# Performance work log

Hardware: AMD Instinct MI355X
Metric: run time of the kernel (lower is better)

Reference implementation:

```python
import math
import jax, jax.numpy as jnp
import numpy as np

# ---- hard-coded constants from the source module ----
T_H = 1.5; M = 60; DT = T_H / M; SQDT = math.sqrt(DT)
ALPHA = 0.8; RHO = 0.3; SQ1MR2 = math.sqrt(1.0 - RHO * RHO)
GAMMA = 5.0; KAPPA_Y = 1.2; LB_W = 1e-3
R = 0.02; SIGMA = 0.2; SIGMA_Y = 0.3; THETA_Y = 0.0; PI_CAP = 2.0
RPTS = 128       # sub_batch (one accumulation iteration)
REPEATS = 128    # total repeats == sub_batch -> single loop pass
N_PTS = 32       # number of eval states
HID = 64


def setup_inputs():
    key = jax.random.key(0)
    ks = jax.random.split(key, 8)
    W = 0.8 + 0.4 * jax.random.uniform(ks[0], (N_PTS, 1), jnp.float32)   # W0_range
    Y = -1.0 + 2.0 * jax.random.uniform(ks[1], (N_PTS, 1), jnp.float32)  # Y0_range
    TmT = jnp.full((N_PTS, 1), T_H, jnp.float32)
    B = RPTS * N_PTS
    # [sim(+/-), draw(z1/z2), step, path, 1] -- fresh noise per antithetic branch, as in torch
    noise = jax.random.normal(ks[2], (2, 2, M, B, 1), jnp.float32)
    w1 = 0.1 * jax.random.normal(ks[3], (3, HID), jnp.float32)
    b1 = jnp.zeros((HID,), jnp.float32)
    w2 = 0.1 * jax.random.normal(ks[4], (HID, HID), jnp.float32)
    b2 = jnp.zeros((HID,), jnp.float32)
    w3 = 0.1 * jax.random.normal(ks[5], (HID, 1), jnp.float32)
    b3 = jnp.zeros((1,), jnp.float32)
    return {"W": W, "TmT": TmT, "Y": Y, "noise": noise,
            "w1": w1, "b1": b1, "w2": w2, "b2": b2, "w3": w3, "b3": b3}


def _policy(params, W, TmT, Y):
    w1, b1, w2, b2, w3, b3 = params
    x = jnp.concatenate([W, TmT, Y], axis=-1)          # [B,3]
    h = jnp.tanh(x @ w1 + b1)
    h = jnp.tanh(h @ w2 + b2)
    return h @ w3 + b3                                 # [B,1]


def _simulate(params, W0, Y0, z1, z2, anti):
    """60-step Euler-Maruyama; returns CRRA utility U(W_T), shape [B,1]."""
    logW = jnp.log(jnp.clip(W0, LB_W, None))
    TmT0 = jnp.full_like(W0, T_H)

    def step(carry, zs):
        logW, Y, TmT = carry
        z1s, z2s = zs
        pi = _policy(params, jnp.exp(logW), TmT, Y)
        zW = anti * z1s
        zY = anti * (RHO * z1s + SQ1MR2 * z2s)
        drift = R + pi * (SIGMA * ALPHA * Y)
        var = (pi * SIGMA) ** 2
        logW = logW + (drift - 0.5 * var) * DT + pi * SIGMA * SQDT * zW
        Y = Y + KAPPA_Y * (THETA_Y - Y) * DT + SIGMA_Y * SQDT * zY
        logW = jnp.log(jnp.clip(jnp.exp(logW), LB_W, None))
        return (logW, Y, TmT - DT), None

    (logW, _, _), _ = jax.lax.scan(step, (logW, Y0, TmT0), (z1, z2))
    W_T = jnp.exp(logW)
    return W_T ** (1.0 - GAMMA) / (1.0 - GAMMA)        # gamma != 1


def reference(W, TmT, Y, noise, w1, b1, w2, b2, w3, b3):
    params = (w1, b1, w2, b2, w3, b3)
    n = W.shape[0]
    Wd = jax.lax.stop_gradient(W)   # forward detaches W, Y
    Yd = jax.lax.stop_gradient(Y)
    W0 = jnp.tile(Wd, (RPTS, 1))    # [B,1]
    Y0 = jnp.tile(Yd, (RPTS, 1))
    z1p, z2p = noise[0, 0], noise[0, 1]
    z1m, z2m = noise[1, 0], noise[1, 1]

    def f(W0_, Y0_):
        U = 0.5 * (_simulate(params, W0_, Y0_, z1p, z2p, 1.0)
                   + _simulate(params, W0_, Y0_, z1m, z2m, -1.0))
        # U_avg.sum() as in torch: mean over rpts, sum over eval points
        return jnp.sum(jnp.mean(U.reshape(RPTS, n), axis=0))

    lam_full = jax.grad(f, 0)(W0, Y0)                  # [B,1]

    def g(W0_, Y0_):
        # lam.view(rpts,n,1).mean(0).sum() == sum(lam_full)/rpts
        return jnp.sum(jax.grad(f, 0)(W0_, Y0_)) / RPTS

    dW_full, dY_full = jax.grad(g, (0, 1))(W0, Y0)     # [B,1] each

    inv = 1.0 / REPEATS   # faithful to source accumulation scaling
    lam = lam_full.reshape(RPTS, n, 1).mean(0) * inv
    dlamW = dW_full.reshape(RPTS, n, 1).mean(0) * inv
    dlamY = dY_full.reshape(RPTS, n, 1).mean(0) * inv

    # project_pmp
    mu_minus_r = SIGMA * (ALPHA * Yd)
    coeff = -1.0 / (Wd * dlamW + 1e-8)
    myo = coeff * (lam * (mu_minus_r / SIGMA ** 2))
    hedge = coeff * (SIGMA * RHO * SIGMA_Y * dlamY / SIGMA ** 2)
    return jnp.clip(myo + hedge, -PI_CAP, PI_CAP)      # [n,1]
```

## Files before the change

kernel.cpp:

```cpp
#include <hip/hip_runtime.h>
#include <math.h>

#define HID    64
#define MSTEPS 60
#define NPTS   32
#define RPTSC  128
#define BTOT   (RPTSC*NPTS)
#define NSIM   (2*BTOT)
#define NWAVE  (NSIM/2)

#define C_DT     0.025f
#define C_SQDT   0.15811388300841897f
#define C_ALPHA  0.8f
#define C_RHO    0.3f
#define C_SQ1MR2 0.9539392014169456f
#define C_KAPPA  1.2f
#define C_R      0.02f
#define C_SIGMA  0.2f
#define C_SIGY   0.3f
#define C_LBW    1e-3f
#define C_LOGLBW -6.907755279f

#define WAVE_LDS 3584
#define A_ROW    144
#define OFF_DV   2304
#define OFF_DA   3328

typedef _Float16 half8 __attribute__((ext_vector_type(8)));
typedef float    f32x4 __attribute__((ext_vector_type(4)));
typedef __fp16   fp16x2 __attribute__((ext_vector_type(2)));

__device__ __forceinline__ float rlanef(float v, int l) {
    return __int_as_float(__builtin_amdgcn_readlane(__float_as_int(v), l));
}
template <int OFF>
__device__ __forceinline__ float swz(float v) {
    return __int_as_float(__builtin_amdgcn_ds_swizzle(__float_as_int(v), OFF));
}
__device__ __forceinline__ f32x4 MFMA(half8 a, half8 b, f32x4 c) {
    return __builtin_amdgcn_mfma_f32_16x16x32_f16(a, b, c, 0, 0, 0);
}
__device__ __forceinline__ float ftanh(float x) {
    float e = __expf(2.0f * x);
    return 1.0f - 2.0f * __builtin_amdgcn_rcpf(e + 1.0f);
}
__device__ __forceinline__ int pk16(float a, float b) {
    return __builtin_bit_cast(int, __builtin_amdgcn_cvt_pkrtz(a, b));
}

__global__ __launch_bounds__(256, 4) void sim_kernel(
    const float* __restrict__ noise,
    const float* __restrict__ w1, const float* __restrict__ b1,
    const float* __restrict__ w2, const float* __restrict__ b2,
    const float* __restrict__ w3, const float* __restrict__ b3,
    const float* __restrict__ Wp, const float* __restrict__ Yp,
    float* __restrict__ sd)
{
    __shared__ __align__(16) char smem[4 * WAVE_LDS];
    const int lane = threadIdx.x & 63;
    const int quad = lane >> 4;
    const int mrow = lane & 15;
    const int par  = lane >> 5;
    char* wb = smem + (threadIdx.x >> 6) * WAVE_LDS;

    const int w = __builtin_amdgcn_readfirstlane(
        (int)((blockIdx.x * blockDim.x + threadIdx.x) >> 6));
    const int simb = w >> 11;
    const int pg   = 2*(w & 2047) + par;
    const int i    = pg & (NPTS - 1);

    const float cW  = w1[lane];
    const float cT  = w1[HID + lane];
    const float cYw = w1[2*HID + lane];
    const float b1k = b1[lane];
    const float b2k = b2[lane];
    const float b3v = b3[0];
    const float cW2  = cW * cW;
    const float cWYc = cW * cYw;

    half8 B00, B01, B02, B03, B10, B11, B12, B13, W30, W31;
    {
        half8 h;
        #define LOADB(dst, q, t) \
            { for (int j = 0; j < 8; ++j) \
                h[j] = (_Float16)w2[((q)*32 + quad*8 + j)*HID + (t)*16 + mrow]; \
              dst = h; }
        LOADB(B00, 0, 0) LOADB(B01, 0, 1) LOADB(B02, 0, 2) LOADB(B03, 0, 3)
        LOADB(B10, 1, 0) LOADB(B11, 1, 1) LOADB(B12, 1, 2) LOADB(B13, 1, 3)
        #undef LOADB
        for (int j = 0; j < 8; ++j) h[j] = (_Float16)w3[0*32 + quad*8 + j];
        W30 = h;
        for (int j = 0; j < 8; ++j) h[j] = (_Float16)w3[1*32 + quad*8 + j];
        W31 = h;
    }

    for (int off = lane*4; off < 16*A_ROW; off += 256)
        *(float*)(wb + off) = 0.0f;

    _Float16* swp = (_Float16*)(wb + lane*2);
    char* arp0 = wb + mrow*A_ROW + quad*16;

    const float* zp1 = noise + (size_t)(simb*2 + 0) * MSTEPS * BTOT + pg;
    const float* zp2 = noise + (size_t)(simb*2 + 1) * MSTEPS * BTOT + pg;

    const float anti = simb ? -1.0f : 1.0f;
    const float ksa  = C_SIGMA * C_ALPHA;
    const float ks2  = C_SIGMA * C_SIGMA;
    const float ksn  = anti * C_SIGMA * C_SQDT;
    const float kFy  = ksa * C_DT;
    const float ksd  = ks2 * C_DT;
    const float kv   = 0.5f * ks2 * C_DT;
    const float kRdt = C_R * C_DT;
    const float ky1  = anti * C_SIGY * C_SQDT * C_RHO;
    const float ky2  = anti * C_SIGY * C_SQDT * C_SQ1MR2;
    const float cYfac = 1.0f - C_KAPPA * C_DT;

    const float W0 = Wp[i];
    float L   = __logf(fmaxf(W0, C_LBW));
    float W   = __expf(L);
    float Yv  = Yp[i];
    float tmt = 1.5f;
    float gW  = 1.0f / W0;
    float hWW = -gW * gW;
    float gY  = 0.0f, hWY = 0.0f;
    float cYt = 1.0f;

    #pragma unroll 1
    for (int m = 0; m < MSTEPS; ++m) {
        asm volatile("" : "+v"(B00), "+v"(B01), "+v"(B02), "+v"(B03),
                          "+v"(B10), "+v"(B11), "+v"(B12), "+v"(B13),
                          "+v"(W30), "+v"(W31));

        const float z1 = zp1[(size_t)m * BTOT];
        const float z2 = zp2[(size_t)m * BTOT];

        const float Wb0 = rlanef(W, 0),  Wb1 = rlanef(W, 32);
        const float Yb0 = rlanef(Yv, 0), Yb1 = rlanef(Yv, 32);

        const float base1 = fmaf(tmt, cT, b1k);
        {
            const float t1 = ftanh(fmaf(Wb0, cW, fmaf(Yb0, cYw, base1)));
            const float dp = 1.0f - t1*t1, ddp = -2.0f*t1*dp;
            swp[0*72] = (_Float16)t1;
            swp[1*72] = (_Float16)(dp * cW);
            swp[2*72] = (_Float16)(dp * cYw);
            swp[3*72] = (_Float16)(ddp * cW2);
            swp[4*72] = (_Float16)(ddp * cWYc);
        }
        {
            const float t1 = ftanh(fmaf(Wb1, cW, fmaf(Yb1, cYw, base1)));
            const float dp = 1.0f - t1*t1, ddp = -2.0f*t1*dp;
            swp[8*72]  = (_Float16)t1;
            swp[9*72]  = (_Float16)(dp * cW);
            swp[10*72] = (_Float16)(dp * cYw);
            swp[11*72] = (_Float16)(ddp * cW2);
            swp[12*72] = (_Float16)(ddp * cWYc);
        }

        half8 af0 = __builtin_bit_cast(half8, *(const f32x4*)arp0);
        half8 af1 = __builtin_bit_cast(half8, *(const f32x4*)(arp0 + 64));

        f32x4 acc[4];
        const f32x4 zz = {0.f, 0.f, 0.f, 0.f};
        acc[0] = MFMA(af1, B10, MFMA(af0, B00, zz));
        acc[1] = MFMA(af1, B11, MFMA(af0, B01, zz));
        acc[2] = MFMA(af1, B12, MFMA(af0, B02, zz));
        acc[3] = MFMA(af1, B13, MFMA(af0, B03, zz));

        {
            const int p = quad >> 1;
            if (!(quad & 1)) {
                #pragma unroll
                for (int t = 0; t < 4; ++t) {
                    int2 v;
                    v.x = pk16(acc[t].x, acc[t].y);
                    v.y = pk16(acc[t].z, acc[t].w);
                    *(int2*)(wb + OFF_DV + (p*64 + t*16 + mrow)*8) = v;
                }
            } else {
                #pragma unroll
                for (int t = 0; t < 4; ++t)
                    *(_Float16*)(wb + OFF_DA + (p*64 + t*16 + mrow)*2) =
                        (_Float16)acc[t].x;
            }
        }

        const int2 dv0 = *(const int2*)(wb + OFF_DV + lane*8);
        const int2 dv1 = *(const int2*)(wb + OFF_DV + (64 + lane)*8);
        const float awy0 = (float)*(const _Float16*)(wb + OFF_DA + lane*2);
        const float awy1 = (float)*(const _Float16*)(wb + OFF_DA + (64 + lane)*2);
        {
            const fp16x2 lo = __builtin_bit_cast(fp16x2, dv0.x);
            const fp16x2 hi = __builtin_bit_cast(fp16x2, dv0.y);
            const float a0 = (float)lo.x, aW = (float)lo.y;
            const float aY = (float)hi.x, aWW = (float)hi.y;
            const float t2 = ftanh(a0 + b2k);
            const float d2 = 1.0f - t2*t2, dd2 = -2.0f*t2*d2;
            const float q  = dd2 * aW;
            swp[0*72] = (_Float16)t2;
            swp[1*72] = (_Float16)(d2 * aW);
            swp[2*72] = (_Float16)(d2 * aY);
            swp[3*72] = (_Float16)fmaf(q, aW, d2 * aWW);
            swp[4*72] = (_Float16)fmaf(q, aY, d2 * awy0);
        }
        {
            const fp16x2 lo = __builtin_bit_cast(fp16x2, dv1.x);
            const fp16x2 hi = __builtin_bit_cast(fp16x2, dv1.y);
            const float a0 = (float)lo.x, aW = (float)lo.y;
            const float aY = (float)hi.x, aWW = (float)hi.y;
            const float t2 = ftanh(a0 + b2k);
            const float d2 = 1.0f - t2*t2, dd2 = -2.0f*t2*d2;
            const float q  = dd2 * aW;
            swp[8*72]  = (_Float16)t2;
            swp[9*72]  = (_Float16)(d2 * aW);
            swp[10*72] = (_Float16)(d2 * aY);
            swp[11*72] = (_Float16)fmaf(q, aW, d2 * aWW);
            swp[12*72] = (_Float16)fmaf(q, aY, d2 * awy1);
        }

        half8 bf0 = __builtin_bit_cast(half8, *(const f32x4*)arp0);
        half8 bf1 = __builtin_bit_cast(half8, *(const f32x4*)(arp0 + 64));
        f32x4 acc4 = MFMA(bf1, W31, MFMA(bf0, W30, zz));

        const float pi  = swz<0x0000>(acc4.x) + b3v;
        const float pW  = swz<0x0000>(acc4.y);
        const float pY  = swz<0x0000>(acc4.z);
        const float pWW = swz<0x0000>(acc4.w);
        const float pWY = swz<0x0200>(acc4.x);

        const float Sn    = ksn * z1;
        const float say   = ksa * Yv;
        const float G     = fmaf(-ks2, pi, say);
        const float GdtSn = fmaf(G, C_DT, Sn);

        const float w2v  = W * W;
        const float piL  = pW * W;
        const float piLL = fmaf(pWW, w2v, piL);
        const float piY  = pY;
        const float piLY = pWY * W;

        const float pi2  = pi * pi;
        const float Lnew = fmaf(pi, fmaf(say, C_DT, Sn),
                                fmaf(-kv, pi2, L + kRdt));

        const float F_L  = fmaf(piL, GdtSn, 1.0f);
        const float F_Y  = fmaf(piY, GdtSn, kFy * pi);
        const float piL2 = piL * piL;
        const float F_LL = fmaf(piLL, GdtSn, -(ksd * piL2));
        const float F_LY = fmaf(piLY, GdtSn, piL * fmaf(-ksd, piY, kFy));

        const float gW2  = gW * gW;
        const float hWWn = fmaf(F_LL, gW2, F_L * hWW);
        const float hWYn = fmaf(F_LL, gW * gY,
                                fmaf(F_LY, gW * cYt, F_L * hWY));
        const float gWn  = F_L * gW;
        const float gYn  = fmaf(F_Y, cYt, F_L * gY);

        Yv  = fmaf(ky2, z2, fmaf(ky1, z1, cYfac * Yv));
        cYt *= cYfac;

        const float We   = __expf(Lnew);
        const bool  clip = (We < C_LBW);
        L   = clip ? C_LOGLBW : Lnew;
        W   = clip ? C_LBW    : We;
        gW  = clip ? 0.0f : gWn;
        gY  = clip ? 0.0f : gYn;
        hWW = clip ? 0.0f : hWWn;
        hWY = clip ? 0.0f : hWYn;
        tmt -= C_DT;
    }

    const float E   = __expf(-4.0f * L);
    const float d1  = E * gW;
    const float d2v = fmaf(-4.0f * E, gW * gW, E * hWW);
    const float d3v = fmaf(-4.0f * E, gW * gY, E * hWY);

    if ((lane & 31) == 0) {
        const int branch = simb * BTOT + pg;
        sd[         branch] = 0.5f * d1;
        sd[  NSIM + branch] = 0.5f * d2v;
        sd[2*NSIM + branch] = 0.5f * d3v;
    }
}

__global__ void proj_kernel(const float* __restrict__ sd,
                            const float* __restrict__ Wp,
                            const float* __restrict__ Yp,
                            float* __restrict__ out)
{
    const int i = threadIdx.x;
    if (i >= NPTS) return;
    float lam = 0.0f, dW = 0.0f, dY = 0.0f;
    #pragma unroll 8
    for (int j = 0; j < NSIM / NPTS; ++j) {
        const int idx = i + (j << 5);
        lam += sd[idx];
        dW  += sd[NSIM + idx];
        dY  += sd[2*NSIM + idx];
    }
    lam *= (1.0f / 2097152.0f);
    dW  *= (1.0f / 268435456.0f);
    dY  *= (1.0f / 268435456.0f);
    const float Wv = Wp[i], Yv = Yp[i];
    const float mmr   = C_SIGMA * (C_ALPHA * Yv);
    const float sig2  = C_SIGMA * C_SIGMA;
    const float coeff = -1.0f / (Wv * dW + 1e-8f);
    const float myo   = coeff * (lam * (mmr / sig2));
    const float hedge = coeff * (C_SIGMA * C_RHO * C_SIGY * dY / sig2);
    float v = myo + hedge;
    v = fminf(fmaxf(v, -2.0f), 2.0f);
    out[i] = v;
}

extern "C" void kernel_launch(void* const* d_in, const int* in_sizes, int n_in,
                              void* d_out, int out_size, void* d_ws, size_t ws_size,
                              hipStream_t stream) {
    const float* Wp    = (const float*)d_in[0];
    const float* Yp    = (const float*)d_in[2];
    const float* noise = (const float*)d_in[3];
    const float* w1    = (const float*)d_in[4];
    const float* b1    = (const float*)d_in[5];
    const float* w2    = (const float*)d_in[6];
    const float* b2    = (const float*)d_in[7];
    const float* w3    = (const float*)d_in[8];
    const float* b3    = (const float*)d_in[9];
    float* out = (float*)d_out;
    float* sd  = (float*)d_ws;

    hipLaunchKernelGGL(sim_kernel, dim3(NWAVE/4), dim3(256), 0, stream,
                       noise, w1, b1, w2, b2, w3, b3, Wp, Yp, sd);
    hipLaunchKernelGGL(proj_kernel, dim3(1), dim3(64), 0, stream, sd, Wp, Yp, out);
}
```

Before: 183.9 us.

## Pack tanh derivative math into fp16x2, fold exp2 scaling, parallelize final reduction

Each lane now processes its two paths' tanh derivative terms together as packed half2 operations. The 2*log2(e) factor is pre-folded into the first-layer weights and biases so tanh uses exp2 directly. The LDS staging layout is interleaved so one 16-byte load plus perm instructions replace two separate loads. The projection kernel becomes a 512-thread two-stage reduction instead of 32 threads looping serially. This cuts VALU work in the per-step critical path, at the cost of lower precision for derivative terms computed in fp16.

```diff
diff --git a/kernel.cpp b/kernel.cpp
--- a/kernel.cpp
+++ b/kernel.cpp
@@ -20,6 +20,7 @@
 #define C_SIGY   0.3f
 #define C_LBW    1e-3f
 #define C_LOGLBW -6.907755279f
+#define C_2L2E   2.8853900817779268f
 
 #define WAVE_LDS 3584
 #define A_ROW    144
@@ -28,7 +29,7 @@
 
 typedef _Float16 half8 __attribute__((ext_vector_type(8)));
 typedef float    f32x4 __attribute__((ext_vector_type(4)));
-typedef __fp16   fp16x2 __attribute__((ext_vector_type(2)));
+typedef _Float16 h2    __attribute__((ext_vector_type(2)));
 
 __device__ __forceinline__ float rlanef(float v, int l) {
     return __int_as_float(__builtin_amdgcn_readlane(__float_as_int(v), l));
@@ -40,12 +41,17 @@
 __device__ __forceinline__ f32x4 MFMA(half8 a, half8 b, f32x4 c) {
     return __builtin_amdgcn_mfma_f32_16x16x32_f16(a, b, c, 0, 0, 0);
 }
-__device__ __forceinline__ float ftanh(float x) {
-    float e = __expf(2.0f * x);
-    return 1.0f - 2.0f * __builtin_amdgcn_rcpf(e + 1.0f);
-}
 __device__ __forceinline__ int pk16(float a, float b) {
     return __builtin_bit_cast(int, __builtin_amdgcn_cvt_pkrtz(a, b));
+}
+__device__ __forceinline__ h2 pk2(float a, float b) {
+    return __builtin_bit_cast(h2, __builtin_amdgcn_cvt_pkrtz(a, b));
+}
+__device__ __forceinline__ h2 permh(unsigned s0, unsigned s1, unsigned sel) {
+    return __builtin_bit_cast(h2, __builtin_amdgcn_perm(s0, s1, sel));
+}
+__device__ __forceinline__ float tanh_fast(float xs) {
+    return 1.0f - 2.0f * __builtin_amdgcn_rcpf(__builtin_amdgcn_exp2f(xs) + 1.0f);
 }
 
 __global__ __launch_bounds__(256, 4) void sim_kernel(
@@ -75,8 +81,17 @@
     const float b1k = b1[lane];
     const float b2k = b2[lane];
     const float b3v = b3[0];
-    const float cW2  = cW * cW;
-    const float cWYc = cW * cYw;
+    const float cW_s  = cW  * C_2L2E;
+    const float cT_s  = cT  * C_2L2E;
+    const float cYw_s = cYw * C_2L2E;
+    const float b1_s  = b1k * C_2L2E;
+    const float b2_s  = b2k * C_2L2E;
+    const h2 cWh  = pk2(cW, cW);
+    const h2 cYwh = pk2(cYw, cYw);
+    const h2 cW2m = pk2(-2.0f*cW*cW,  -2.0f*cW*cW);
+    const h2 cWYm = pk2(-2.0f*cW*cYw, -2.0f*cW*cYw);
+    const h2 hone = {(_Float16)1.0f,  (_Float16)1.0f};
+    const h2 m2h  = {(_Float16)-2.0f, (_Float16)-2.0f};
 
     half8 B00, B01, B02, B03, B10, B11, B12, B13, W30, W31;
     {
@@ -137,24 +152,22 @@
         const float Wb0 = rlanef(W, 0),  Wb1 = rlanef(W, 32);
         const float Yb0 = rlanef(Yv, 0), Yb1 = rlanef(Yv, 32);
 
-        const float base1 = fmaf(tmt, cT, b1k);
+        const float base1s = fmaf(tmt, cT_s, b1_s);
         {
-            const float t1 = ftanh(fmaf(Wb0, cW, fmaf(Yb0, cYw, base1)));
-            const float dp = 1.0f - t1*t1, ddp = -2.0f*t1*dp;
-            swp[0*72] = (_Float16)t1;
-            swp[1*72] = (_Float16)(dp * cW);
-            swp[2*72] = (_Float16)(dp * cYw);
-            swp[3*72] = (_Float16)(ddp * cW2);
-            swp[4*72] = (_Float16)(ddp * cWYc);
-        }
-        {
-            const float t1 = ftanh(fmaf(Wb1, cW, fmaf(Yb1, cYw, base1)));
-            const float dp = 1.0f - t1*t1, ddp = -2.0f*t1*dp;
-            swp[8*72]  = (_Float16)t1;
-            swp[9*72]  = (_Float16)(dp * cW);
-            swp[10*72] = (_Float16)(dp * cYw);
-            swp[11*72] = (_Float16)(ddp * cW2);
-            swp[12*72] = (_Float16)(ddp * cWYc);
+            const float t10 = tanh_fast(fmaf(Wb0, cW_s, fmaf(Yb0, cYw_s, base1s)));
+            const float t11 = tanh_fast(fmaf(Wb1, cW_s, fmaf(Yb1, cYw_s, base1s)));
+            const h2 tp  = pk2(t10, t11);
+            const h2 dpp = hone - tp * tp;
+            const h2 ddq = tp * dpp;
+            const h2 r1 = dpp * cWh;
+            const h2 r2 = dpp * cYwh;
+            const h2 r3 = ddq * cW2m;
+            const h2 r4 = ddq * cWYm;
+            swp[0*72] = tp.x;  swp[8*72]  = tp.y;
+            swp[1*72] = r1.x;  swp[9*72]  = r1.y;
+            swp[2*72] = r2.x;  swp[10*72] = r2.y;
+            swp[3*72] = r3.x;  swp[11*72] = r3.y;
+            swp[4*72] = r4.x;  swp[12*72] = r4.y;
         }
 
         half8 af0 = __builtin_bit_cast(half8, *(const f32x4*)arp0);
@@ -175,47 +188,42 @@
                     int2 v;
                     v.x = pk16(acc[t].x, acc[t].y);
                     v.y = pk16(acc[t].z, acc[t].w);
-                    *(int2*)(wb + OFF_DV + (p*64 + t*16 + mrow)*8) = v;
+                    *(int2*)(wb + OFF_DV + ((t*16 + mrow) << 4) + (p << 3)) = v;
                 }
             } else {
                 #pragma unroll
                 for (int t = 0; t < 4; ++t)
-                    *(_Float16*)(wb + OFF_DA + (p*64 + t*16 + mrow)*2) =
+                    *(_Float16*)(wb + OFF_DA + ((t*16 + mrow) << 2) + (p << 1)) =
                         (_Float16)acc[t].x;
             }
         }
 
-        const int2 dv0 = *(const int2*)(wb + OFF_DV + lane*8);
-        const int2 dv1 = *(const int2*)(wb + OFF_DV + (64 + lane)*8);
-        const float awy0 = (float)*(const _Float16*)(wb + OFF_DA + lane*2);
-        const float awy1 = (float)*(const _Float16*)(wb + OFF_DA + (64 + lane)*2);
+        const f32x4 dvv = *(const f32x4*)(wb + OFF_DV + lane*16);
+        const h2 awyp   = *(const h2*)(wb + OFF_DA + lane*4);
         {
-            const fp16x2 lo = __builtin_bit_cast(fp16x2, dv0.x);
-            const fp16x2 hi = __builtin_bit_cast(fp16x2, dv0.y);
-            const float a0 = (float)lo.x, aW = (float)lo.y;
-            const float aY = (float)hi.x, aWW = (float)hi.y;
-            const float t2 = ftanh(a0 + b2k);
-            const float d2 = 1.0f - t2*t2, dd2 = -2.0f*t2*d2;
-            const float q  = dd2 * aW;
-            swp[0*72] = (_Float16)t2;
-            swp[1*72] = (_Float16)(d2 * aW);
-            swp[2*72] = (_Float16)(d2 * aY);
-            swp[3*72] = (_Float16)fmaf(q, aW, d2 * aWW);
-            swp[4*72] = (_Float16)fmaf(q, aY, d2 * awy0);
-        }
-        {
-            const fp16x2 lo = __builtin_bit_cast(fp16x2, dv1.x);
-            const fp16x2 hi = __builtin_bit_cast(fp16x2, dv1.y);
-            const float a0 = (float)lo.x, aW = (float)lo.y;
-            const float aY = (float)hi.x, aWW = (float)hi.y;
-            const float t2 = ftanh(a0 + b2k);
-            const float d2 = 1.0f - t2*t2, dd2 = -2.0f*t2*d2;
-            const float q  = dd2 * aW;
-            swp[8*72]  = (_Float16)t2;
-            swp[9*72]  = (_Float16)(d2 * aW);
-            swp[10*72] = (_Float16)(d2 * aY);
-            swp[11*72] = (_Float16)fmaf(q, aW, d2 * aWW);
-            swp[12*72] = (_Float16)fmaf(q, aY, d2 * awy1);
+            const unsigned q0 = __builtin_bit_cast(unsigned, dvv.x);
+            const unsigned q1 = __builtin_bit_cast(unsigned, dvv.y);
+            const unsigned q2 = __builtin_bit_cast(unsigned, dvv.z);
+            const unsigned q3 = __builtin_bit_cast(unsigned, dvv.w);
+            const h2 a0p  = permh(q2, q0, 0x05040100);
+            const h2 aWp  = permh(q2, q0, 0x07060302);
+            const h2 aYp  = permh(q3, q1, 0x05040100);
+            const h2 aWWp = permh(q3, q1, 0x07060302);
+
+            const float t20 = tanh_fast(fmaf((float)a0p.x, C_2L2E, b2_s));
+            const float t21 = tanh_fast(fmaf((float)a0p.y, C_2L2E, b2_s));
+            const h2 t2p = pk2(t20, t21);
+            const h2 d2p = hone - t2p * t2p;
+            const h2 qp  = (m2h * (t2p * d2p)) * aWp;
+            const h2 s1 = d2p * aWp;
+            const h2 s2 = d2p * aYp;
+            const h2 s3 = qp * aWp + d2p * aWWp;
+            const h2 s4 = qp * aYp + d2p * awyp;
+            swp[0*72] = t2p.x; swp[8*72]  = t2p.y;
+            swp[1*72] = s1.x;  swp[9*72]  = s1.y;
+            swp[2*72] = s2.x;  swp[10*72] = s2.y;
+            swp[3*72] = s3.x;  swp[11*72] = s3.y;
+            swp[4*72] = s4.x;  swp[12*72] = s4.y;
         }
 
         half8 bf0 = __builtin_bit_cast(half8, *(const f32x4*)arp0);
@@ -283,33 +291,47 @@
     }
 }
 
-__global__ void proj_kernel(const float* __restrict__ sd,
-                            const float* __restrict__ Wp,
-                            const float* __restrict__ Yp,
-                            float* __restrict__ out)
+__global__ __launch_bounds__(512) void proj_kernel(
+    const float* __restrict__ sd,
+    const float* __restrict__ Wp,
+    const float* __restrict__ Yp,
+    float* __restrict__ out)
 {
-    const int i = threadIdx.x;
-    if (i >= NPTS) return;
-    float lam = 0.0f, dW = 0.0f, dY = 0.0f;
-    #pragma unroll 8
-    for (int j = 0; j < NSIM / NPTS; ++j) {
-        const int idx = i + (j << 5);
+    __shared__ float red[3 * 512];
+    const int tid = threadIdx.x;
+    const int i = tid & 31;
+    const int c = tid >> 5;
+    float lam = 0.f, dW = 0.f, dY = 0.f;
+    #pragma unroll 4
+    for (int jj = 0; jj < 16; ++jj) {
+        const int idx = i + ((jj*16 + c) << 5);
         lam += sd[idx];
         dW  += sd[NSIM + idx];
         dY  += sd[2*NSIM + idx];
     }
-    lam *= (1.0f / 2097152.0f);
-    dW  *= (1.0f / 268435456.0f);
-    dY  *= (1.0f / 268435456.0f);
-    const float Wv = Wp[i], Yv = Yp[i];
-    const float mmr   = C_SIGMA * (C_ALPHA * Yv);
-    const float sig2  = C_SIGMA * C_SIGMA;
-    const float coeff = -1.0f / (Wv * dW + 1e-8f);
-    const float myo   = coeff * (lam * (mmr / sig2));
-    const float hedge = coeff * (C_SIGMA * C_RHO * C_SIGY * dY / sig2);
-    float v = myo + hedge;
-    v = fminf(fmaxf(v, -2.0f), 2.0f);
-    out[i] = v;
+    red[tid] = lam; red[512 + tid] = dW; red[1024 + tid] = dY;
+    __syncthreads();
+    if (tid < NPTS) {
+        float l = 0.f, w = 0.f, y = 0.f;
+        #pragma unroll
+        for (int c2 = 0; c2 < 16; ++c2) {
+            l += red[c2*32 + i];
+            w += red[512 + c2*32 + i];
+            y += red[1024 + c2*32 + i];
+        }
+        l *= (1.0f / 2097152.0f);
+        w *= (1.0f / 268435456.0f);
+        y *= (1.0f / 268435456.0f);
+        const float Wv = Wp[i], Yv = Yp[i];
+        const float mmr   = C_SIGMA * (C_ALPHA * Yv);
+        const float sig2  = C_SIGMA * C_SIGMA;
+        const float coeff = -1.0f / (Wv * w + 1e-8f);
+        const float myo   = coeff * (l * (mmr / sig2));
+        const float hedge = coeff * (C_SIGMA * C_RHO * C_SIGY * y / sig2);
+        float v = myo + hedge;
+        v = fminf(fmaxf(v, -2.0f), 2.0f);
+        out[i] = v;
+    }
 }
 
 extern "C" void kernel_launch(void* const* d_in, const int* in_sizes, int n_in,
@@ -329,5 +351,5 @@
 
     hipLaunchKernelGGL(sim_kernel, dim3(NWAVE/4), dim3(256), 0, stream,
                        noise, w1, b1, w2, b2, w3, b3, Wp, Yp, sd);
-    hipLaunchKernelGGL(proj_kernel, dim3(1), dim3(64), 0, stream, sd, Wp, Yp, out);
-}
+    hipLaunchKernelGGL(proj_kernel, dim3(1), dim3(512), 0, stream, sd, Wp, Yp, out);
+}
```

After: 163.0 us. -11.4%, faster.
